# Performance work log

Measured on AMD Instinct MI355X. Metric: run time of the kernel, lower is better.

## Reference

```python
import jax, jax.numpy as jnp
import numpy as np

N = 50000      # nodes
E = 800000     # directed edges (before self-loops)
IN = 128       # in_channels
H = 4          # heads (layers 1,2)
C = 64         # hidden_channels per head
OUT = 512      # out_channels of final Linear
LEAKY_SLOPE = 0.2


def _gat_layer(x, src, dst, n, W, a_src, a_dst, b, concat):
    """PyG GATConv (v1): shared linear, additive attention, segment softmax over dst."""
    heads, ch = a_src.shape
    xl = (x @ W).reshape(n, heads, ch)                       # [N,H,C]
    as_n = jnp.sum(xl * a_src, axis=-1)                      # [N,H] alpha_src per node
    ad_n = jnp.sum(xl * a_dst, axis=-1)                      # [N,H] alpha_dst per node
    logits = jax.nn.leaky_relu(as_n[src] + ad_n[dst], LEAKY_SLOPE)  # [Etot,H]
    m = jax.lax.stop_gradient(jax.ops.segment_max(logits, dst, num_segments=n))
    p = jnp.exp(logits - m[dst])
    denom = jax.ops.segment_sum(p, dst, num_segments=n) + 1e-16
    alpha = p / denom[dst]                                   # segment softmax over incoming edges
    out = jax.ops.segment_sum(xl[src] * alpha[:, :, None], dst, num_segments=n)  # [N,H,C]
    out = out.reshape(n, heads * ch) if concat else out.mean(axis=1)
    return out + b


def setup_inputs() -> dict:
    key = jax.random.key(0)
    ks = jax.random.split(key, 16)

    def gl(k, shape, fan_in):
        return jax.random.normal(k, shape, dtype=jnp.float32) * np.float32(1.0 / np.sqrt(fan_in))

    x = jax.random.normal(ks[0], (N, IN), dtype=jnp.float32)
    edge_index = jax.random.randint(ks[1], (2, E), 0, N, dtype=jnp.int32)

    inp = {
        "x": x,
        "edge_index": edge_index,
        # layer 1: in -> H*C (concat)
        "W1": gl(ks[2], (IN, H * C), IN),
        "a_src1": gl(ks[3], (H, C), C),
        "a_dst1": gl(ks[4], (H, C), C),
        "b1": jnp.zeros((H * C,), jnp.float32),
        # layer 2: H*C -> H*C (concat)
        "W2": gl(ks[5], (H * C, H * C), H * C),
        "a_src2": gl(ks[6], (H, C), C),
        "a_dst2": gl(ks[7], (H, C), C),
        "b2": jnp.zeros((H * C,), jnp.float32),
        # layer 3: H*C -> C (1 head, no concat)
        "W3": gl(ks[8], (H * C, C), H * C),
        "a_src3": gl(ks[9], (1, C), C),
        "a_dst3": gl(ks[10], (1, C), C),
        "b3": jnp.zeros((C,), jnp.float32),
        # final fc: C -> OUT
        "Wfc": gl(ks[11], (C, OUT), C),
        "bfc": jnp.zeros((OUT,), jnp.float32),
    }
    return inp


def reference(x, edge_index, W1, a_src1, a_dst1, b1, W2, a_src2, a_dst2, b2,
              W3, a_src3, a_dst3, b3, Wfc, bfc):
    n = x.shape[0]
    loop = jnp.arange(n, dtype=edge_index.dtype)             # PyG GATConv adds self-loops
    src = jnp.concatenate([edge_index[0], loop])
    dst = jnp.concatenate([edge_index[1], loop])

    h = jax.nn.relu(_gat_layer(x, src, dst, n, W1, a_src1, a_dst1, b1, True))
    h = jax.nn.relu(_gat_layer(h, src, dst, n, W2, a_src2, a_dst2, b2, True))
    h = jax.nn.relu(_gat_layer(h, src, dst, n, W3, a_src3, a_dst3, b3, False))
    return jax.nn.relu(h @ Wfc + bfc)                        # [N, OUT]
```

## Files before the change

kernel.cpp:

```cpp
#include <hip/hip_runtime.h>
#include <cstdint>
#include <cstddef>

typedef unsigned short ushort_t;
typedef __bf16 bf16x8 __attribute__((ext_vector_type(8)));
typedef float f32x4 __attribute__((ext_vector_type(4)));

__device__ __forceinline__ float b2f(ushort_t u) {
    return __uint_as_float(((unsigned int)u) << 16);
}
__device__ __forceinline__ ushort_t f2b(float f) {
    __bf16 h = (__bf16)f;
    return *(ushort_t*)&h;
}

__device__ __forceinline__ void stage8(const float* __restrict__ g, ushort_t* s) {
    float4 f0 = *(const float4*)g;
    float4 f1 = *(const float4*)(g + 4);
    union { ushort_t u[8]; uint4 v; } t;
    t.u[0] = f2b(f0.x); t.u[1] = f2b(f0.y); t.u[2] = f2b(f0.z); t.u[3] = f2b(f0.w);
    t.u[4] = f2b(f1.x); t.u[5] = f2b(f1.y); t.u[6] = f2b(f1.z); t.u[7] = f2b(f1.w);
    *(uint4*)s = t.v;
}
__device__ __forceinline__ void stage8(const ushort_t* __restrict__ g, ushort_t* s) {
    *(float4*)s = *(const float4*)g;
}

__global__ __launch_bounds__(256) void transpose_kernel(const float* __restrict__ W,
                                                        ushort_t* __restrict__ WT,
                                                        int K, int N2) {
    int id = blockIdx.x * 256 + threadIdx.x;
    if (id >= K * N2) return;
    int n = id / K, k = id - n * K;
    WT[id] = f2b(W[k * N2 + n]);
}

__global__ __launch_bounds__(256) void degree_kernel(const int* __restrict__ ei_dst,
                                                     int* __restrict__ deg, int E, int Etot) {
    int e = blockIdx.x * 256 + threadIdx.x;
    if (e >= Etot) return;
    int d = (e < E) ? ei_dst[e] : (e - E);
    atomicAdd(&deg[d], 1);
}

__global__ __launch_bounds__(256) void partial_sum_kernel(const int* __restrict__ deg,
                                                          int* __restrict__ bsum, int n) {
    __shared__ int ws[4];
    int t = threadIdx.x;
    int i = blockIdx.x * 256 + t;
    int v = (i < n) ? deg[i] : 0;
#pragma unroll
    for (int off = 32; off; off >>= 1) v += __shfl_xor(v, off, 64);
    if ((t & 63) == 0) ws[t >> 6] = v;
    __syncthreads();
    if (t == 0) bsum[blockIdx.x] = ws[0] + ws[1] + ws[2] + ws[3];
}

__global__ __launch_bounds__(256) void scan_bsum_kernel(const int* __restrict__ bsum,
                                                        int* __restrict__ boff,
                                                        int* __restrict__ rowoff,
                                                        int nblk, int n) {
    __shared__ int sm[256];
    int t = threadIdx.x;
    int v = (t < nblk) ? bsum[t] : 0;
    sm[t] = v;
    __syncthreads();
#pragma unroll
    for (int off = 1; off < 256; off <<= 1) {
        int u = (t >= off) ? sm[t - off] : 0;
        __syncthreads();
        sm[t] += u;
        __syncthreads();
    }
    if (t < nblk) boff[t] = sm[t] - v;
    if (t == 255) rowoff[n] = sm[255];
}

__global__ __launch_bounds__(256) void block_scan_kernel(const int* __restrict__ deg,
                                                         const int* __restrict__ boff,
                                                         int* __restrict__ rowoff, int n) {
    __shared__ int sm[256];
    int t = threadIdx.x;
    int i = blockIdx.x * 256 + t;
    int v = (i < n) ? deg[i] : 0;
    sm[t] = v;
    __syncthreads();
#pragma unroll
    for (int off = 1; off < 256; off <<= 1) {
        int u = (t >= off) ? sm[t - off] : 0;
        __syncthreads();
        sm[t] += u;
        __syncthreads();
    }
    if (i < n) rowoff[i] = boff[blockIdx.x] + sm[t] - v;
}

__global__ __launch_bounds__(256) void copy_cursor_kernel(const int* __restrict__ rowoff,
                                                          int* __restrict__ cursor, int n) {
    int i = blockIdx.x * 256 + threadIdx.x;
    if (i < n) cursor[i] = rowoff[i];
}

__global__ __launch_bounds__(256) void fill_sdst_kernel(const int* __restrict__ rowoff,
                                                        int* __restrict__ sdst, int n) {
    int d = blockIdx.x * 256 + threadIdx.x;
    if (d >= n) return;
    int a = rowoff[d], b = rowoff[d + 1];
    for (int i = a; i < b; i++) sdst[i] = d;
}

__global__ __launch_bounds__(256) void scatter_kernel(const int* __restrict__ ei_src,
                                                      const int* __restrict__ ei_dst,
                                                      int* __restrict__ cursor,
                                                      int* __restrict__ ssrc, int E, int Etot) {
    int e = blockIdx.x * 256 + threadIdx.x;
    if (e >= Etot) return;
    int s, d;
    if (e < E) { s = ei_src[e]; d = ei_dst[e]; } else { s = d = e - E; }
    int pos = atomicAdd(&cursor[d], 1);
    ssrc[pos] = s;
}

template <int H>
__global__ __launch_bounds__(256) void edge_p_kernel(const int* __restrict__ ssrc,
                                                     const int* __restrict__ sdst,
                                                     const float* __restrict__ as_n,
                                                     const float* __restrict__ ad_n,
                                                     float* __restrict__ p, int Etot) {
    int id = blockIdx.x * 256 + threadIdx.x;
    if (H == 4) {
        if (id >= Etot * 4) return;
        int e = id >> 2, h = id & 3;
        int s = ssrc[e], d = sdst[e];
        float lg = as_n[s * 4 + h] + ad_n[d * 4 + h];
        lg = lg > 0.f ? lg : 0.2f * lg;
        p[id] = __expf(lg);
    } else {
        if (id >= Etot) return;
        int s = ssrc[id], d = sdst[id];
        float lg = as_n[s] + ad_n[d];
        lg = lg > 0.f ? lg : 0.2f * lg;
        p[id] = __expf(lg);
    }
}

template <typename TA, bool EPI>
__global__ __launch_bounds__(256) void gemm_mfma(const TA* __restrict__ A,
                                                 const ushort_t* __restrict__ WT,
                                                 float* __restrict__ C,
                                                 ushort_t* __restrict__ Cb,
                                                 const float* __restrict__ bias,
                                                 int M, int K, int N2) {
    __shared__ ushort_t sA[64 * 32];
    __shared__ ushort_t sB[64 * 32];
    const int tid = threadIdx.x;
    const int wv = tid >> 6, lane = tid & 63;
    const int quad = lane >> 4, l16 = lane & 15;
    const int bm = blockIdx.x * 64, bn = blockIdx.y * 64;
    const int srow = tid >> 2, skof = (tid & 3) * 8;
    f32x4 acc[4] = {};

    for (int k0 = 0; k0 < K; k0 += 32) {
        int gm = bm + srow;
        gm = gm < M ? gm : M - 1;
        stage8(A + (size_t)gm * K + k0 + skof, sA + srow * 32 + skof);
        stage8(WT + (size_t)(bn + srow) * K + k0 + skof, sB + srow * 32 + skof);
        __syncthreads();

        bf16x8 af = *(const bf16x8*)(sA + (wv * 16 + l16) * 32 + quad * 8);
#pragma unroll
        for (int j = 0; j < 4; j++) {
            bf16x8 bf = *(const bf16x8*)(sB + (j * 16 + l16) * 32 + quad * 8);
            acc[j] = __builtin_amdgcn_mfma_f32_16x16x32_bf16(af, bf, acc[j], 0, 0, 0);
        }
        __syncthreads();
    }

#pragma unroll
    for (int j = 0; j < 4; j++) {
        int col = bn + j * 16 + l16;
        float bv = EPI ? bias[col] : 0.f;
#pragma unroll
        for (int r = 0; r < 4; r++) {
            int row = bm + wv * 16 + quad * 4 + r;
            if (row < M) {
                float v = acc[j][r];
                if (EPI) {
                    v += bv;
                    v = v > 0.f ? v : 0.f;
                    C[(size_t)row * N2 + col] = v;
                } else {
                    Cb[(size_t)row * N2 + col] = f2b(v);
                }
            }
        }
    }
}

template <int CH>
__global__ __launch_bounds__(256) void attn_kernel(const ushort_t* __restrict__ xl,
                                                   const float* __restrict__ a_src,
                                                   const float* __restrict__ a_dst,
                                                   float* __restrict__ as_n,
                                                   float* __restrict__ ad_n, int N) {
    int n = blockIdx.x * 4 + (threadIdx.x >> 6);
    int lane = threadIdx.x & 63;
    if (n >= N) return;
    if (CH == 256) {
        ushort4 u = ((const ushort4*)xl)[(size_t)n * 64 + lane];
        float4 av = ((const float4*)a_src)[lane];
        float4 dv = ((const float4*)a_dst)[lane];
        float x0 = b2f(u.x), x1 = b2f(u.y), x2 = b2f(u.z), x3 = b2f(u.w);
        float s = x0 * av.x + x1 * av.y + x2 * av.z + x3 * av.w;
        float d = x0 * dv.x + x1 * dv.y + x2 * dv.z + x3 * dv.w;
#pragma unroll
        for (int off = 8; off; off >>= 1) {
            s += __shfl_xor(s, off, 64);
            d += __shfl_xor(d, off, 64);
        }
        if ((lane & 15) == 0) {
            int h = lane >> 4;
            as_n[n * 4 + h] = s;
            ad_n[n * 4 + h] = d;
        }
    } else {
        float xv = b2f(xl[(size_t)n * 64 + lane]);
        float s = xv * a_src[lane];
        float d = xv * a_dst[lane];
#pragma unroll
        for (int off = 32; off; off >>= 1) {
            s += __shfl_xor(s, off, 64);
            d += __shfl_xor(d, off, 64);
        }
        if (lane == 0) { as_n[n] = s; ad_n[n] = d; }
    }
}

template <int CH>
__global__ __launch_bounds__(256) void aggregate_kernel(const ushort_t* __restrict__ xl,
                                                        const float* __restrict__ pp,
                                                        const int* __restrict__ rowoff,
                                                        const int* __restrict__ ssrc,
                                                        const float* __restrict__ bias,
                                                        ushort_t* __restrict__ hout, int N) {
    int dd = blockIdx.x * 4 + (threadIdx.x >> 6);
    int lane = threadIdx.x & 63;
    if (dd >= N) return;
    int r0 = rowoff[dd], r1 = rowoff[dd + 1];
    if (CH == 256) {
        const int h = lane >> 4;
        const ushort4* xv = (const ushort4*)xl;
        float a0 = 0.f, a1 = 0.f, a2 = 0.f, a3 = 0.f, den = 0.f;
        for (int i = r0; i < r1; i += 8) {
            int idx[8];
            float pv[8];
            ushort4 u[8];
#pragma unroll
            for (int j = 0; j < 8; j++) {
                int t = i + j;
                int id2 = t < r1 ? t : r0;
                idx[j] = ssrc[id2];
                float pw = pp[id2 * 4 + h];
                pv[j] = t < r1 ? pw : 0.f;
            }
#pragma unroll
            for (int j = 0; j < 8; j++) u[j] = xv[(size_t)idx[j] * 64 + lane];
#pragma unroll
            for (int j = 0; j < 8; j++) {
                den += pv[j];
                a0 += pv[j] * b2f(u[j].x);
                a1 += pv[j] * b2f(u[j].y);
                a2 += pv[j] * b2f(u[j].z);
                a3 += pv[j] * b2f(u[j].w);
            }
        }
        float di = 1.f / (den + 1e-16f);
        float4 bv = ((const float4*)bias)[lane];
        float v0 = a0 * di + bv.x;
        float v1 = a1 * di + bv.y;
        float v2 = a2 * di + bv.z;
        float v3 = a3 * di + bv.w;
        ushort4 o;
        o.x = f2b(v0 > 0.f ? v0 : 0.f);
        o.y = f2b(v1 > 0.f ? v1 : 0.f);
        o.z = f2b(v2 > 0.f ? v2 : 0.f);
        o.w = f2b(v3 > 0.f ? v3 : 0.f);
        ((ushort4*)hout)[(size_t)dd * 64 + lane] = o;
    } else {
        float a0 = 0.f, den = 0.f;
        for (int i = r0; i < r1; i += 8) {
            int idx[8];
            float pv[8];
            ushort_t u[8];
#pragma unroll
            for (int j = 0; j < 8; j++) {
                int t = i + j;
                int id2 = t < r1 ? t : r0;
                idx[j] = ssrc[id2];
                float pw = pp[id2];
                pv[j] = t < r1 ? pw : 0.f;
            }
#pragma unroll
            for (int j = 0; j < 8; j++) u[j] = xl[(size_t)idx[j] * 64 + lane];
#pragma unroll
            for (int j = 0; j < 8; j++) {
                den += pv[j];
                a0 += pv[j] * b2f(u[j]);
            }
        }
        float v = a0 / (den + 1e-16f) + bias[lane];
        hout[(size_t)dd * 64 + lane] = f2b(v > 0.f ? v : 0.f);
    }
}

extern "C" void kernel_launch(void* const* d_in, const int* in_sizes, int n_in,
                              void* d_out, int out_size, void* d_ws, size_t ws_size,
                              hipStream_t stream) {
    const int N = in_sizes[0] / 128;
    const int E = in_sizes[1] / 2;
    const int Etot = E + N;

    const float* x = (const float*)d_in[0];
    const int* ei = (const int*)d_in[1];
    const int* ei_src = ei;
    const int* ei_dst = ei + E;
    float* out = (float*)d_out;

    const float* as1 = (const float*)d_in[3];
    const float* ad1 = (const float*)d_in[4];
    const float* b1  = (const float*)d_in[5];
    const float* as2 = (const float*)d_in[7];
    const float* ad2 = (const float*)d_in[8];
    const float* b2  = (const float*)d_in[9];
    const float* as3 = (const float*)d_in[11];
    const float* ad3 = (const float*)d_in[12];
    const float* b3  = (const float*)d_in[13];
    const float* bfc = (const float*)d_in[15];

    ushort_t* bufX = (ushort_t*)d_ws;
    ushort_t* bufH = bufX + (size_t)N * 256;
    ushort_t* W1T  = bufH + (size_t)N * 256;
    ushort_t* W2T  = W1T + 32768;
    ushort_t* W3T  = W2T + 65536;
    ushort_t* WfcT = W3T + 16384;
    float* asn = (float*)(WfcT + 32768);
    float* adn = asn + (size_t)N * 4;
    int* deg    = (int*)(adn + (size_t)N * 4);
    int* rowoff = deg + N;
    int* cursor = rowoff + N + 1;
    int* ssrc   = cursor + N;
    int* sdst   = ssrc + Etot;
    int* bsum   = sdst + Etot;
    int* boff   = bsum + 256;
    float* pbuf = (float*)(boff + 256);

    transpose_kernel<<<(128 * 256 + 255) / 256, 256, 0, stream>>>((const float*)d_in[2], W1T, 128, 256);
    transpose_kernel<<<(256 * 256 + 255) / 256, 256, 0, stream>>>((const float*)d_in[6], W2T, 256, 256);
    transpose_kernel<<<(256 * 64 + 255) / 256, 256, 0, stream>>>((const float*)d_in[10], W3T, 256, 64);
    transpose_kernel<<<(64 * 512 + 255) / 256, 256, 0, stream>>>((const float*)d_in[14], WfcT, 64, 512);

    hipMemsetAsync(deg, 0, (size_t)N * sizeof(int), stream);
    int eb = (Etot + 255) / 256;
    degree_kernel<<<eb, 256, 0, stream>>>(ei_dst, deg, E, Etot);
    const int NBLK = (N + 255) / 256;
    partial_sum_kernel<<<NBLK, 256, 0, stream>>>(deg, bsum, N);
    scan_bsum_kernel<<<1, 256, 0, stream>>>(bsum, boff, rowoff, NBLK, N);
    block_scan_kernel<<<NBLK, 256, 0, stream>>>(deg, boff, rowoff, N);
    copy_cursor_kernel<<<NBLK, 256, 0, stream>>>(rowoff, cursor, N);
    fill_sdst_kernel<<<NBLK, 256, 0, stream>>>(rowoff, sdst, N);
    scatter_kernel<<<eb, 256, 0, stream>>>(ei_src, ei_dst, cursor, ssrc, E, Etot);

    const int MB = (N + 63) / 64;
    int nb4 = (N + 3) / 4;
    int epb4 = (Etot * 4 + 255) / 256;
    int epb1 = (Etot + 255) / 256;

    gemm_mfma<float, false><<<dim3(MB, 4), 256, 0, stream>>>(x, W1T, nullptr, bufX, nullptr, N, 128, 256);
    attn_kernel<256><<<nb4, 256, 0, stream>>>(bufX, as1, ad1, asn, adn, N);
    edge_p_kernel<4><<<epb4, 256, 0, stream>>>(ssrc, sdst, asn, adn, pbuf, Etot);
    aggregate_kernel<256><<<nb4, 256, 0, stream>>>(bufX, pbuf, rowoff, ssrc, b1, bufH, N);

    gemm_mfma<ushort_t, false><<<dim3(MB, 4), 256, 0, stream>>>(bufH, W2T, nullptr, bufX, nullptr, N, 256, 256);
    attn_kernel<256><<<nb4, 256, 0, stream>>>(bufX, as2, ad2, asn, adn, N);
    edge_p_kernel<4><<<epb4, 256, 0, stream>>>(ssrc, sdst, asn, adn, pbuf, Etot);
    aggregate_kernel<256><<<nb4, 256, 0, stream>>>(bufX, pbuf, rowoff, ssrc, b2, bufH, N);

    gemm_mfma<ushort_t, false><<<dim3(MB, 1), 256, 0, stream>>>(bufH, W3T, nullptr, bufX, nullptr, N, 256, 64);
    attn_kernel<64><<<nb4, 256, 0, stream>>>(bufX, as3, ad3, asn, adn, N);
    edge_p_kernel<1><<<epb1, 256, 0, stream>>>(ssrc, sdst, asn, adn, pbuf, Etot);
    aggregate_kernel<64><<<nb4, 256, 0, stream>>>(bufX, pbuf, rowoff, ssrc, b3, bufH, N);

    gemm_mfma<ushort_t, true><<<dim3(MB, 8), 256, 0, stream>>>(bufH, WfcT, out, nullptr, bfc, N, 64, 512);
}
```

Measured before the change: 529.4 us.

## Fuse edge attention logits into aggregation and widen per-lane loads

Removes the separate edge_p kernels, the sdst fill kernel and the per-edge p buffer, computing leaky-relu and exp of the attention logits inline inside the aggregation loop from per-node alpha_src/alpha_dst. Aggregation is also remapped so each lane loads 8 bf16 values (uint4), giving two destination nodes per wave for 256 channels and eight per wave for 64 channels. This drops several launches and the write and re-read of an edge-sized buffer, at the cost of recomputing exp for every channel lane and a gather of as_n per edge.

Result: faster. 496.7 us (-6.2%).

```diff
diff --git a/kernel.cpp b/kernel.cpp
--- a/kernel.cpp
+++ b/kernel.cpp
@@ -12,6 +12,11 @@
 __device__ __forceinline__ ushort_t f2b(float f) {
     __bf16 h = (__bf16)f;
     return *(ushort_t*)&h;
+}
+__device__ __forceinline__ float lo16(unsigned int u) { return __uint_as_float(u << 16); }
+__device__ __forceinline__ float hi16(unsigned int u) { return __uint_as_float(u & 0xffff0000u); }
+__device__ __forceinline__ unsigned int pack2(float a, float b) {
+    return ((unsigned int)f2b(b) << 16) | (unsigned int)f2b(a);
 }
 
 __device__ __forceinline__ void stage8(const float* __restrict__ g, ushort_t* s) {
@@ -99,14 +104,6 @@
                                                           int* __restrict__ cursor, int n) {
     int i = blockIdx.x * 256 + threadIdx.x;
     if (i < n) cursor[i] = rowoff[i];
-}
-
-__global__ __launch_bounds__(256) void fill_sdst_kernel(const int* __restrict__ rowoff,
-                                                        int* __restrict__ sdst, int n) {
-    int d = blockIdx.x * 256 + threadIdx.x;
-    if (d >= n) return;
-    int a = rowoff[d], b = rowoff[d + 1];
-    for (int i = a; i < b; i++) sdst[i] = d;
 }
 
 __global__ __launch_bounds__(256) void scatter_kernel(const int* __restrict__ ei_src,
@@ -119,29 +116,6 @@
     if (e < E) { s = ei_src[e]; d = ei_dst[e]; } else { s = d = e - E; }
     int pos = atomicAdd(&cursor[d], 1);
     ssrc[pos] = s;
-}
-
-template <int H>
-__global__ __launch_bounds__(256) void edge_p_kernel(const int* __restrict__ ssrc,
-                                                     const int* __restrict__ sdst,
-                                                     const float* __restrict__ as_n,
-                                                     const float* __restrict__ ad_n,
-                                                     float* __restrict__ p, int Etot) {
-    int id = blockIdx.x * 256 + threadIdx.x;
-    if (H == 4) {
-        if (id >= Etot * 4) return;
-        int e = id >> 2, h = id & 3;
-        int s = ssrc[e], d = sdst[e];
-        float lg = as_n[s * 4 + h] + ad_n[d * 4 + h];
-        lg = lg > 0.f ? lg : 0.2f * lg;
-        p[id] = __expf(lg);
-    } else {
-        if (id >= Etot) return;
-        int s = ssrc[id], d = sdst[id];
-        float lg = as_n[s] + ad_n[d];
-        lg = lg > 0.f ? lg : 0.2f * lg;
-        p[id] = __expf(lg);
-    }
 }
 
 template <typename TA, bool EPI>
@@ -238,78 +212,110 @@
 
 template <int CH>
 __global__ __launch_bounds__(256) void aggregate_kernel(const ushort_t* __restrict__ xl,
-                                                        const float* __restrict__ pp,
+                                                        const float* __restrict__ as_n,
+                                                        const float* __restrict__ ad_n,
                                                         const int* __restrict__ rowoff,
                                                         const int* __restrict__ ssrc,
                                                         const float* __restrict__ bias,
                                                         ushort_t* __restrict__ hout, int N) {
-    int dd = blockIdx.x * 4 + (threadIdx.x >> 6);
-    int lane = threadIdx.x & 63;
-    if (dd >= N) return;
-    int r0 = rowoff[dd], r1 = rowoff[dd + 1];
+    const int tid = threadIdx.x;
+    const int wv = tid >> 6, lane = tid & 63;
+    const uint4* xv = (const uint4*)xl;
     if (CH == 256) {
-        const int h = lane >> 4;
-        const ushort4* xv = (const ushort4*)xl;
-        float a0 = 0.f, a1 = 0.f, a2 = 0.f, a3 = 0.f, den = 0.f;
+        const int hw = lane >> 5, l32 = lane & 31;
+        const int dd = blockIdx.x * 8 + wv * 2 + hw;
+        if (dd >= N) return;
+        const int h = l32 >> 3;
+        const int r0 = rowoff[dd], r1 = rowoff[dd + 1];
+        const float adv = ad_n[dd * 4 + h];
+        float a0 = 0, a1 = 0, a2 = 0, a3 = 0, a4 = 0, a5 = 0, a6 = 0, a7 = 0, den = 0;
         for (int i = r0; i < r1; i += 8) {
-            int idx[8];
-            float pv[8];
-            ushort4 u[8];
+            int s[8];
+            float g[8];
+            uint4 u[8];
 #pragma unroll
             for (int j = 0; j < 8; j++) {
                 int t = i + j;
-                int id2 = t < r1 ? t : r0;
-                idx[j] = ssrc[id2];
-                float pw = pp[id2 * 4 + h];
-                pv[j] = t < r1 ? pw : 0.f;
-            }
-#pragma unroll
-            for (int j = 0; j < 8; j++) u[j] = xv[(size_t)idx[j] * 64 + lane];
+                s[j] = ssrc[t < r1 ? t : r0];
+            }
+#pragma unroll
+            for (int j = 0; j < 8; j++) g[j] = as_n[s[j] * 4 + h];
+#pragma unroll
+            for (int j = 0; j < 8; j++) u[j] = xv[(size_t)s[j] * 32 + l32];
 #pragma unroll
             for (int j = 0; j < 8; j++) {
-                den += pv[j];
-                a0 += pv[j] * b2f(u[j].x);
-                a1 += pv[j] * b2f(u[j].y);
-                a2 += pv[j] * b2f(u[j].z);
-                a3 += pv[j] * b2f(u[j].w);
+                float lg = g[j] + adv;
+                lg = lg > 0.f ? lg : 0.2f * lg;
+                float p = (i + j < r1) ? __expf(lg) : 0.f;
+                den += p;
+                a0 += p * lo16(u[j].x); a1 += p * hi16(u[j].x);
+                a2 += p * lo16(u[j].y); a3 += p * hi16(u[j].y);
+                a4 += p * lo16(u[j].z); a5 += p * hi16(u[j].z);
+                a6 += p * lo16(u[j].w); a7 += p * hi16(u[j].w);
             }
         }
         float di = 1.f / (den + 1e-16f);
-        float4 bv = ((const float4*)bias)[lane];
-        float v0 = a0 * di + bv.x;
-        float v1 = a1 * di + bv.y;
-        float v2 = a2 * di + bv.z;
-        float v3 = a3 * di + bv.w;
-        ushort4 o;
-        o.x = f2b(v0 > 0.f ? v0 : 0.f);
-        o.y = f2b(v1 > 0.f ? v1 : 0.f);
-        o.z = f2b(v2 > 0.f ? v2 : 0.f);
-        o.w = f2b(v3 > 0.f ? v3 : 0.f);
-        ((ushort4*)hout)[(size_t)dd * 64 + lane] = o;
+        float4 b0 = ((const float4*)bias)[l32 * 2];
+        float4 b1 = ((const float4*)bias)[l32 * 2 + 1];
+        float v0 = a0 * di + b0.x, v1 = a1 * di + b0.y;
+        float v2 = a2 * di + b0.z, v3 = a3 * di + b0.w;
+        float v4 = a4 * di + b1.x, v5 = a5 * di + b1.y;
+        float v6 = a6 * di + b1.z, v7 = a7 * di + b1.w;
+        v0 = v0 > 0.f ? v0 : 0.f; v1 = v1 > 0.f ? v1 : 0.f;
+        v2 = v2 > 0.f ? v2 : 0.f; v3 = v3 > 0.f ? v3 : 0.f;
+        v4 = v4 > 0.f ? v4 : 0.f; v5 = v5 > 0.f ? v5 : 0.f;
+        v6 = v6 > 0.f ? v6 : 0.f; v7 = v7 > 0.f ? v7 : 0.f;
+        uint4 o;
+        o.x = pack2(v0, v1); o.y = pack2(v2, v3);
+        o.z = pack2(v4, v5); o.w = pack2(v6, v7);
+        ((uint4*)hout)[(size_t)dd * 32 + l32] = o;
     } else {
-        float a0 = 0.f, den = 0.f;
+        const int grp = lane >> 3, l8 = lane & 7;
+        const int dd = blockIdx.x * 32 + wv * 8 + grp;
+        if (dd >= N) return;
+        const int r0 = rowoff[dd], r1 = rowoff[dd + 1];
+        const float adv = ad_n[dd];
+        float a0 = 0, a1 = 0, a2 = 0, a3 = 0, a4 = 0, a5 = 0, a6 = 0, a7 = 0, den = 0;
         for (int i = r0; i < r1; i += 8) {
-            int idx[8];
-            float pv[8];
-            ushort_t u[8];
+            int s[8];
+            float g[8];
+            uint4 u[8];
 #pragma unroll
             for (int j = 0; j < 8; j++) {
                 int t = i + j;
-                int id2 = t < r1 ? t : r0;
-                idx[j] = ssrc[id2];
-                float pw = pp[id2];
-                pv[j] = t < r1 ? pw : 0.f;
-            }
-#pragma unroll
-            for (int j = 0; j < 8; j++) u[j] = xl[(size_t)idx[j] * 64 + lane];
+                s[j] = ssrc[t < r1 ? t : r0];
+            }
+#pragma unroll
+            for (int j = 0; j < 8; j++) g[j] = as_n[s[j]];
+#pragma unroll
+            for (int j = 0; j < 8; j++) u[j] = xv[(size_t)s[j] * 8 + l8];
 #pragma unroll
             for (int j = 0; j < 8; j++) {
-                den += pv[j];
-                a0 += pv[j] * b2f(u[j]);
-            }
-        }
-        float v = a0 / (den + 1e-16f) + bias[lane];
-        hout[(size_t)dd * 64 + lane] = f2b(v > 0.f ? v : 0.f);
+                float lg = g[j] + adv;
+                lg = lg > 0.f ? lg : 0.2f * lg;
+                float p = (i + j < r1) ? __expf(lg) : 0.f;
+                den += p;
+                a0 += p * lo16(u[j].x); a1 += p * hi16(u[j].x);
+                a2 += p * lo16(u[j].y); a3 += p * hi16(u[j].y);
+                a4 += p * lo16(u[j].z); a5 += p * hi16(u[j].z);
+                a6 += p * lo16(u[j].w); a7 += p * hi16(u[j].w);
+            }
+        }
+        float di = 1.f / (den + 1e-16f);
+        float4 b0 = ((const float4*)bias)[l8 * 2];
+        float4 b1 = ((const float4*)bias)[l8 * 2 + 1];
+        float v0 = a0 * di + b0.x, v1 = a1 * di + b0.y;
+        float v2 = a2 * di + b0.z, v3 = a3 * di + b0.w;
+        float v4 = a4 * di + b1.x, v5 = a5 * di + b1.y;
+        float v6 = a6 * di + b1.z, v7 = a7 * di + b1.w;
+        v0 = v0 > 0.f ? v0 : 0.f; v1 = v1 > 0.f ? v1 : 0.f;
+        v2 = v2 > 0.f ? v2 : 0.f; v3 = v3 > 0.f ? v3 : 0.f;
+        v4 = v4 > 0.f ? v4 : 0.f; v5 = v5 > 0.f ? v5 : 0.f;
+        v6 = v6 > 0.f ? v6 : 0.f; v7 = v7 > 0.f ? v7 : 0.f;
+        uint4 o;
+        o.x = pack2(v0, v1); o.y = pack2(v2, v3);
+        o.z = pack2(v4, v5); o.w = pack2(v6, v7);
+        ((uint4*)hout)[(size_t)dd * 8 + l8] = o;
     }
 }
 
@@ -349,10 +355,8 @@
     int* rowoff = deg + N;
     int* cursor = rowoff + N + 1;
     int* ssrc   = cursor + N;
-    int* sdst   = ssrc + Etot;
-    int* bsum   = sdst + Etot;
+    int* bsum   = ssrc + Etot;
     int* boff   = bsum + 256;
-    float* pbuf = (float*)(boff + 256);
 
     transpose_kernel<<<(128 * 256 + 255) / 256, 256, 0, stream>>>((const float*)d_in[2], W1T, 128, 256);
     transpose_kernel<<<(256 * 256 + 255) / 256, 256, 0, stream>>>((const float*)d_in[6], W2T, 256, 256);
@@ -367,28 +371,24 @@
     scan_bsum_kernel<<<1, 256, 0, stream>>>(bsum, boff, rowoff, NBLK, N);
     block_scan_kernel<<<NBLK, 256, 0, stream>>>(deg, boff, rowoff, N);
     copy_cursor_kernel<<<NBLK, 256, 0, stream>>>(rowoff, cursor, N);
-    fill_sdst_kernel<<<NBLK, 256, 0, stream>>>(rowoff, sdst, N);
     scatter_kernel<<<eb, 256, 0, stream>>>(ei_src, ei_dst, cursor, ssrc, E, Etot);
 
     const int MB = (N + 63) / 64;
     int nb4 = (N + 3) / 4;
-    int epb4 = (Etot * 4 + 255) / 256;
-    int epb1 = (Etot + 255) / 256;
+    int nb8 = (N + 7) / 8;
+    int nb32 = (N + 31) / 32;
 
     gemm_mfma<float, false><<<dim3(MB, 4), 256, 0, stream>>>(x, W1T, nullptr, bufX, nullptr, N, 128, 256);
     attn_kernel<256><<<nb4, 256, 0, stream>>>(bufX, as1, ad1, asn, adn, N);
-    edge_p_kernel<4><<<epb4, 256, 0, stream>>>(ssrc, sdst, asn, adn, pbuf, Etot);
-    aggregate_kernel<256><<<nb4, 256, 0, stream>>>(bufX, pbuf, rowoff, ssrc, b1, bufH, N);
+    aggregate_kernel<256><<<nb8, 256, 0, stream>>>(bufX, asn, adn, rowoff, ssrc, b1, bufH, N);
 
     gemm_mfma<ushort_t, false><<<dim3(MB, 4), 256, 0, stream>>>(bufH, W2T, nullptr, bufX, nullptr, N, 256, 256);
     attn_kernel<256><<<nb4, 256, 0, stream>>>(bufX, as2, ad2, asn, adn, N);
-    edge_p_kernel<4><<<epb4, 256, 0, stream>>>(ssrc, sdst, asn, adn, pbuf, Etot);
-    aggregate_kernel<256><<<nb4, 256, 0, stream>>>(bufX, pbuf, rowoff, ssrc, b2, bufH, N);
+    aggregate_kernel<256><<<nb8, 256, 0, stream>>>(bufX, asn, adn, rowoff, ssrc, b2, bufH, N);
 
     gemm_mfma<ushort_t, false><<<dim3(MB, 1), 256, 0, stream>>>(bufH, W3T, nullptr, bufX, nullptr, N, 256, 64);
     attn_kernel<64><<<nb4, 256, 0, stream>>>(bufX, as3, ad3, asn, adn, N);
-    edge_p_kernel<1><<<epb1, 256, 0, stream>>>(ssrc, sdst, asn, adn, pbuf, Etot);
-    aggregate_kernel<64><<<nb4, 256, 0, stream>>>(bufX, pbuf, rowoff, ssrc, b3, bufH, N);
+    aggregate_kernel<64><<<nb32, 256, 0, stream>>>(bufX, asn, adn, rowoff, ssrc, b3, bufH, N);
 
     gemm_mfma<ushort_t, true><<<dim3(MB, 8), 256, 0, stream>>>(bufH, WfcT, out, nullptr, bfc, N, 64, 512);
 }
```
